# Kernel tuning notes

Hardware: AMD Instinct MI355X
Metric: run time of the kernel (lower is better)

The kernel has to match this reference:

```python
import jax, jax.numpy as jnp
import numpy as np
from jax import lax

C = 256
HEADS = 8
HEAD_DIM = C // HEADS
B, H, W = 16, 32, 32
EPS = 1e-5


def conv3x3(x, w, b):
    # x: [B,C,H,W], w: [O,I,3,3]
    y = lax.conv_general_dilated(x, w, (1, 1), 'SAME',
                                 dimension_numbers=('NCHW', 'OIHW', 'NCHW'))
    return y + b[None, :, None, None]


def conv1x1(x, w, b):
    # w: [O,C]; pointwise conv as einsum
    return jnp.einsum('oc,bchw->bohw', w, x) + b[None, :, None, None]


def batchnorm(x, gamma, beta, mean, var):
    inv = gamma / jnp.sqrt(var + EPS)
    return x * inv[None, :, None, None] + (beta - mean * inv)[None, :, None, None]


def setup_inputs() -> dict:
    key = jax.random.key(0)
    ks = jax.random.split(key, 16)
    s3 = 1.0 / np.sqrt(C * 9)
    s1 = 1.0 / np.sqrt(C)
    return {
        'x': jax.random.normal(ks[0], (B, C, H, W), jnp.float32),
        'conv1_w': jax.random.normal(ks[1], (C, C, 3, 3), jnp.float32) * s3,
        'conv1_b': jnp.zeros((C,), jnp.float32),
        'bn1_gamma': jnp.ones((C,), jnp.float32),
        'bn1_beta': jnp.zeros((C,), jnp.float32),
        'bn1_mean': jax.random.normal(ks[2], (C,), jnp.float32) * 0.1,
        'bn1_var': jax.random.uniform(ks[3], (C,), jnp.float32, 0.5, 1.5),
        'conv2_w': jax.random.normal(ks[4], (C, C, 3, 3), jnp.float32) * s3,
        'conv2_b': jnp.zeros((C,), jnp.float32),
        'bn2_gamma': jnp.ones((C,), jnp.float32),
        'bn2_beta': jnp.zeros((C,), jnp.float32),
        'bn2_mean': jax.random.normal(ks[5], (C,), jnp.float32) * 0.1,
        'bn2_var': jax.random.uniform(ks[6], (C,), jnp.float32, 0.5, 1.5),
        'q_w': jax.random.normal(ks[7], (C, C), jnp.float32) * s1,
        'q_b': jnp.zeros((C,), jnp.float32),
        'k_w': jax.random.normal(ks[8], (C, C), jnp.float32) * s1,
        'k_b': jnp.zeros((C,), jnp.float32),
        'v_w': jax.random.normal(ks[9], (C, C), jnp.float32) * s1,
        'v_b': jnp.zeros((C,), jnp.float32),
        'out_w': jax.random.normal(ks[10], (C, C), jnp.float32) * s1,
        'out_b': jnp.zeros((C,), jnp.float32),
        'gate': jnp.asarray(0.1, jnp.float32),
    }


def reference(x, conv1_w, conv1_b, bn1_gamma, bn1_beta, bn1_mean, bn1_var,
              conv2_w, conv2_b, bn2_gamma, bn2_beta, bn2_mean, bn2_var,
              q_w, q_b, k_w, k_b, v_w, v_b, out_w, out_b, gate):
    b, c, h, w = x.shape
    n = h * w
    residual = x
    # conv residual path
    conv_out = jax.nn.relu(batchnorm(conv3x3(x, conv1_w, conv1_b),
                                     bn1_gamma, bn1_beta, bn1_mean, bn1_var))
    conv_out = batchnorm(conv3x3(conv_out, conv2_w, conv2_b),
                         bn2_gamma, bn2_beta, bn2_mean, bn2_var)
    # spatial multi-head attention (eval mode: dropout is identity)
    q = conv1x1(x, q_w, q_b).reshape(b, HEADS, HEAD_DIM, n)
    k = conv1x1(x, k_w, k_b).reshape(b, HEADS, HEAD_DIM, n)
    v = conv1x1(x, v_w, v_b).reshape(b, HEADS, HEAD_DIM, n)
    scores = jnp.einsum('bhdn,bhdm->bhnm', q, k) / np.sqrt(HEAD_DIM).astype(np.float32)
    attn = jax.nn.softmax(scores, axis=-1)  # [B,heads,N,N]
    attn_out = jnp.einsum('bhdm,bhnm->bhdn', v, attn).reshape(b, c, h, w)
    attn_out = conv1x1(attn_out, out_w, out_b)
    out = conv_out + jax.nn.sigmoid(gate) * attn_out + residual
    return jax.nn.relu(out)
```

## Files before the change

kernel.cpp:

```cpp
#include <hip/hip_runtime.h>
#include <hip/hip_bf16.h>

using bf16 = __hip_bfloat16;
typedef __attribute__((ext_vector_type(4))) float floatx4;
typedef __attribute__((ext_vector_type(8))) __bf16 bf16x8;
typedef __attribute__((ext_vector_type(4))) __bf16 bf16x4;

#define LGKM_WAIT() asm volatile("s_waitcnt lgkmcnt(0)" ::: "memory")

__device__ __forceinline__ void prep_one(const float* __restrict__ src,
                                         bf16* __restrict__ dst, int idx, int ntaps)
{
    const int kk = idx & 31, o = (idx >> 5) & 255, kc = (idx >> 13) & 7, t = idx >> 16;
    dst[idx] = __float2bfloat16(src[(o * 256 + kc * 32 + kk) * ntaps + t]);
}

__global__ __launch_bounds__(256) void prep_all(
    const float* __restrict__ x,
    const float* __restrict__ w1, const float* __restrict__ w2,
    const float* __restrict__ qw, const float* __restrict__ kw,
    const float* __restrict__ vw, const float* __restrict__ ow,
    bf16* __restrict__ xk, bf16* __restrict__ w1f, bf16* __restrict__ w2f,
    bf16* __restrict__ qwf, bf16* __restrict__ kwf,
    bf16* __restrict__ vwf, bf16* __restrict__ owf)
{
    __shared__ float T[64][65];
    const int blk = blockIdx.x, tid = threadIdx.x;
    if (blk < 1024) {
        const int n0 = (blk & 15) * 64, c0 = ((blk >> 4) & 3) * 64, b = blk >> 6;
        #pragma unroll
        for (int it = 0; it < 4; ++it) {
            const int tau = tid + it * 256;
            const int c = tau >> 4, seg = tau & 15;
            const float4 vv = *(const float4*)&x[((b * 256 + c0 + c) << 10) + n0 + seg * 4];
            T[seg * 4 + 0][c] = vv.x; T[seg * 4 + 1][c] = vv.y;
            T[seg * 4 + 2][c] = vv.z; T[seg * 4 + 3][c] = vv.w;
        }
        __syncthreads();
        #pragma unroll
        for (int it = 0; it < 2; ++it) {
            const int tau = tid + it * 256;
            const int n = tau >> 3, seg = tau & 7;
            bf16x8 o8;
            #pragma unroll
            for (int q = 0; q < 8; ++q) o8[q] = (__bf16)T[n][seg * 8 + q];
            const int c = c0 + seg * 8;
            *(bf16x8*)&xk[((((b << 3) + (c >> 5)) << 10) + n0 + n) * 32 + (c & 31)] = o8;
        }
    } else if (blk < 2176) {
        const int base = (blk - 1024) * 256 + tid;
        #pragma unroll
        for (int k = 0; k < 4; ++k) {
            const int idx = base + k * 294912;
            if (idx < 589824) prep_one(w1, w1f, idx, 9);
            else              prep_one(w2, w2f, idx - 589824, 9);
        }
    } else {
        const int r = (blk - 2176) * 256 + tid;
        prep_one(qw, qwf, r, 1);
        prep_one(kw, kwf, r, 1);
        prep_one(vw, vwf, r, 1);
        prep_one(ow, owf, r, 1);
    }
}

template<int MODE>
__global__ __launch_bounds__(256) void conv_k(
    const bf16* __restrict__ Wf, const bf16* __restrict__ Act,
    const float* __restrict__ bias,
    const float* __restrict__ gam, const float* __restrict__ bet,
    const float* __restrict__ mu, const float* __restrict__ var,
    void* __restrict__ outp)
{
    __shared__ __align__(16) unsigned char smb[34816];

    const int bn = blockIdx.x, bo = blockIdx.y, b = blockIdx.z;
    const int tid = threadIdx.x;
    const int wave = tid >> 6, lane = tid & 63;
    const int quad = lane >> 4, l16 = lane & 15;
    const int wm = wave & 1, wn = wave >> 1;

    int srow[4], scol[4], sn[4]; bool sval[4];
    #pragma unroll
    for (int it = 0; it < 4; ++it) {
        const int s = tid + it * 256;
        const int row = s >> 2;
        const int yi = row / 34, x34 = row - yi * 34;
        const int gy = bn * 4 - 1 + yi, gx = x34 - 1;
        sval[it] = (s < 816) & (gy >= 0) & (gy < 32) & (gx >= 0) & (gx < 32);
        sn[it] = (gy << 5) + gx;
        srow[it] = row; scol[it] = (s & 3) * 8;
    }

    const bf16* __restrict__ act0 = Act + ((size_t)b << 18);
    bf16x8 rg[4];
    #pragma unroll
    for (int it = 0; it < 4; ++it) {
        bf16x8 v = {};
        if (sval[it]) v = *(const bf16x8*)&act0[sn[it] * 32 + scol[it]];
        rg[it] = v;
    }
    {
        bf16* st = (bf16*)smb;
        #pragma unroll
        for (int it = 0; it < 4; ++it)
            if (tid + it * 256 < 816) *(bf16x8*)&st[srow[it] * 40 + scol[it]] = rg[it];
    }
    __syncthreads();

    floatx4 acc[4][2] = {};

    for (int kc = 0; kc < 8; ++kc) {
        if (kc < 7) {
            const bf16* __restrict__ actn = act0 + ((kc + 1) << 15);
            #pragma unroll
            for (int it = 0; it < 4; ++it) {
                bf16x8 v = {};
                if (sval[it]) v = *(const bf16x8*)&actn[sn[it] * 32 + scol[it]];
                rg[it] = v;
            }
        }
        const bf16* __restrict__ cur = (const bf16*)(smb + (kc & 1) * 16320);
        #pragma unroll
        for (int t = 0; t < 9; ++t) {
            const int dy = t / 3 - 1, dx = t % 3 - 1;
            bf16x8 af[4], wf[2];
            #pragma unroll
            for (int p = 0; p < 4; ++p) {
                const int m = wm * 64 + p * 16 + l16;
                const int row = ((m >> 5) + 1 + dy) * 34 + ((m & 31) + 1 + dx);
                af[p] = *(const bf16x8*)&cur[row * 40 + quad * 8];
            }
            #pragma unroll
            for (int p = 0; p < 2; ++p)
                wf[p] = *(const bf16x8*)&Wf[((((t * 8 + kc) << 8) + bo * 64 + wn * 32 + p * 16 + l16) << 5) + quad * 8];
            #pragma unroll
            for (int i = 0; i < 4; ++i)
                #pragma unroll
                for (int j = 0; j < 2; ++j)
                    acc[i][j] = __builtin_amdgcn_mfma_f32_16x16x32_bf16(af[i], wf[j], acc[i][j], 0, 0, 0);
        }
        if (kc < 7) {
            bf16* nxt = (bf16*)(smb + ((kc + 1) & 1) * 16320);
            #pragma unroll
            for (int it = 0; it < 4; ++it)
                if (tid + it * 256 < 816) *(bf16x8*)&nxt[srow[it] * 40 + scol[it]] = rg[it];
        }
        __syncthreads();
    }

    if constexpr (MODE == 0) {
        bf16* rp = (bf16*)(smb + wave * 5120);
        #pragma unroll
        for (int i = 0; i < 4; ++i)
            #pragma unroll
            for (int j = 0; j < 2; ++j) {
                const int oc = bo * 64 + wn * 32 + j * 16 + l16;
                const float inv = gam[oc] * rsqrtf(var[oc] + 1e-5f);
                const float sh = bet[oc] - mu[oc] * inv;
                const float bs = bias[oc];
                #pragma unroll
                for (int r = 0; r < 4; ++r) {
                    const float v = (acc[i][j][r] + bs) * inv + sh;
                    rp[(i * 16 + quad * 4 + r) * 40 + j * 16 + l16] =
                        __float2bfloat16(v < 0.0f ? 0.0f : v);
                }
            }
        LGKM_WAIT();
        const int kc2 = bo * 2 + wn;
        bf16* dst = (bf16*)outp + ((((size_t)b << 3) + kc2) << 15) + (bn * 128 + wm * 64) * 32;
        #pragma unroll
        for (int it = 0; it < 4; ++it) {
            const int s = it * 64 + lane;
            const int nl = s >> 2, cp = (s & 3) * 8;
            *(bf16x8*)&dst[nl * 32 + cp] = *(const bf16x8*)&rp[nl * 40 + cp];
        }
    } else {
        float* rp = (float*)(smb + wave * 8704);
        #pragma unroll
        for (int i = 0; i < 4; ++i)
            #pragma unroll
            for (int j = 0; j < 2; ++j) {
                const int oc = bo * 64 + wn * 32 + j * 16 + l16;
                const float inv = gam[oc] * rsqrtf(var[oc] + 1e-5f);
                const float sh = bet[oc] - mu[oc] * inv;
                const float bs = bias[oc];
                float4 o;
                o.x = (acc[i][j][0] + bs) * inv + sh;
                o.y = (acc[i][j][1] + bs) * inv + sh;
                o.z = (acc[i][j][2] + bs) * inv + sh;
                o.w = (acc[i][j][3] + bs) * inv + sh;
                *(float4*)&rp[(j * 16 + l16) * 68 + i * 16 + quad * 4] = o;
            }
        LGKM_WAIT();
        const int n0 = bn * 128 + wm * 64;
        #pragma unroll
        for (int it = 0; it < 8; ++it) {
            const int s = it * 64 + lane;
            const int ocl = s >> 4, nch = s & 15;
            const int oc = bo * 64 + wn * 32 + ocl;
            float4 v = *(const float4*)&rp[ocl * 68 + nch * 4];
            *(float4*)&((float*)outp)[((b * 256 + oc) << 10) + n0 + nch * 4] = v;
        }
    }
}

__global__ __launch_bounds__(256) void qkv_k(
    const bf16* __restrict__ Wq, const bf16* __restrict__ Wk, const bf16* __restrict__ Wv,
    const bf16* __restrict__ Act,
    const float* __restrict__ bq, const float* __restrict__ bk, const float* __restrict__ bv,
    bf16* __restrict__ Oq, bf16* __restrict__ Ok, bf16* __restrict__ Ov, float qscale)
{
    __shared__ __align__(16) unsigned char qsm[20480];
    const int bn = blockIdx.x, by = blockIdx.y, b = blockIdx.z;
    const int sel = by >> 2, bo = by & 3;
    const bf16* __restrict__ Wf = (sel == 0) ? Wq : (sel == 1) ? Wk : Wv;
    const float* __restrict__ bias = (sel == 0) ? bq : (sel == 1) ? bk : bv;
    const float scale = (sel == 0) ? qscale : 1.0f;

    const int tid = threadIdx.x;
    const int wave = tid >> 6, lane = tid & 63;
    const int quad = lane >> 4, l16 = lane & 15;
    const int wm = wave & 1, wn = wave >> 1;

    floatx4 acc[4][2] = {};

    for (int kc = 0; kc < 8; ++kc) {
        const bf16* __restrict__ actk = Act + ((size_t)b << 18) + (kc << 15);
        bf16x8 af[4], wf[2];
        #pragma unroll
        for (int p = 0; p < 4; ++p)
            af[p] = *(const bf16x8*)&actk[(bn * 128 + wm * 64 + p * 16 + l16) * 32 + quad * 8];
        #pragma unroll
        for (int p = 0; p < 2; ++p)
            wf[p] = *(const bf16x8*)&Wf[(((kc << 8) + bo * 64 + wn * 32 + p * 16 + l16) << 5) + quad * 8];
        #pragma unroll
        for (int i = 0; i < 4; ++i)
            #pragma unroll
            for (int j = 0; j < 2; ++j)
                acc[i][j] = __builtin_amdgcn_mfma_f32_16x16x32_bf16(af[i], wf[j], acc[i][j], 0, 0, 0);
    }

    if (sel < 2) {
        bf16* rp = (bf16*)(qsm + wave * 5120);
        #pragma unroll
        for (int i = 0; i < 4; ++i)
            #pragma unroll
            for (int j = 0; j < 2; ++j) {
                const int oc = bo * 64 + wn * 32 + j * 16 + l16;
                const float bs = bias[oc];
                #pragma unroll
                for (int r = 0; r < 4; ++r)
                    rp[(i * 16 + quad * 4 + r) * 40 + j * 16 + l16] =
                        __float2bfloat16((acc[i][j][r] + bs) * scale);
            }
        LGKM_WAIT();
        bf16* __restrict__ outp = (sel == 0) ? Oq : Ok;
        const int h = bo * 2 + wn;
        bf16* dst = outp + ((((size_t)b << 3) + h) << 15) + (bn * 128 + wm * 64) * 32;
        #pragma unroll
        for (int it = 0; it < 4; ++it) {
            const int s = it * 64 + lane;
            const int nl = s >> 2, cp = (s & 3) * 8;
            *(bf16x8*)&dst[nl * 32 + cp] = *(const bf16x8*)&rp[nl * 40 + cp];
        }
    } else {
        bf16* rp = (bf16*)(qsm + wave * 4608);
        #pragma unroll
        for (int i = 0; i < 4; ++i)
            #pragma unroll
            for (int j = 0; j < 2; ++j) {
                const int oc = bo * 64 + wn * 32 + j * 16 + l16;
                const float bs = bias[oc];
                bf16x4 o4;
                #pragma unroll
                for (int r = 0; r < 4; ++r) o4[r] = (__bf16)(acc[i][j][r] + bs);
                *(bf16x4*)&rp[(j * 16 + l16) * 72 + i * 16 + quad * 4] = o4;
            }
        LGKM_WAIT();
        const int n0 = bn * 128 + wm * 64;
        #pragma unroll
        for (int it = 0; it < 4; ++it) {
            const int s = it * 64 + lane;
            const int ocl = s >> 3, nch = s & 7;
            const int oc = bo * 64 + wn * 32 + ocl;
            *(bf16x8*)&Ov[((b * 256 + oc) << 10) + n0 + nch * 8] =
                *(const bf16x8*)&rp[ocl * 72 + nch * 8];
        }
    }
}

__global__ __launch_bounds__(256) void attn_kernel(
    const bf16* __restrict__ Q, const bf16* __restrict__ K,
    const bf16* __restrict__ V, bf16* __restrict__ O)
{
    __shared__ __align__(16) bf16 Pl[4][32][136];

    const int qb = blockIdx.x, h = blockIdx.y, b = blockIdx.z;
    const int tid = threadIdx.x;
    const int wave = tid >> 6, lane = tid & 63;
    const int quad = lane >> 4, l16 = lane & 15;

    const bf16* __restrict__ Qh = Q + ((((size_t)b << 3) + h) << 15);
    const bf16* __restrict__ Kh = K + ((((size_t)b << 3) + h) << 15);
    const int qrow0 = qb * 128 + wave * 32;

    bf16x8 qf[2];
    #pragma unroll
    for (int i = 0; i < 2; ++i)
        qf[i] = *(const bf16x8*)&Qh[(qrow0 + i * 16 + l16) * 32 + quad * 8];

    float lp[2] = {0.0f, 0.0f};
    floatx4 oacc[2][2] = {};

    for (int kt = 0; kt < 8; ++kt) {
        bf16x8 kf[8];
        #pragma unroll
        for (int kb = 0; kb < 8; ++kb)
            kf[kb] = *(const bf16x8*)&Kh[(kt * 128 + kb * 16 + l16) * 32 + quad * 8];
        bf16x8 vb[2][4];
        #pragma unroll
        for (int jd = 0; jd < 2; ++jd)
            #pragma unroll
            for (int kk = 0; kk < 4; ++kk)
                vb[jd][kk] = *(const bf16x8*)&V[((b * 256 + h * 32 + jd * 16 + l16) << 10)
                                               + kt * 128 + kk * 32 + quad * 8];

        #pragma unroll
        for (int kb = 0; kb < 8; ++kb) {
            #pragma unroll
            for (int i = 0; i < 2; ++i) {
                floatx4 zz = {0.f, 0.f, 0.f, 0.f};
                floatx4 st = __builtin_amdgcn_mfma_f32_16x16x32_bf16(kf[kb], qf[i], zz, 0, 0, 0);
                const float e0 = __expf(st[0]), e1 = __expf(st[1]);
                const float e2 = __expf(st[2]), e3 = __expf(st[3]);
                lp[i] += (e0 + e1) + (e2 + e3);
                bf16x4 p4 = {(__bf16)e0, (__bf16)e1, (__bf16)e2, (__bf16)e3};
                *(bf16x4*)&Pl[wave][i * 16 + l16][kb * 16 + quad * 4] = p4;
            }
        }

        #pragma unroll
        for (int kk = 0; kk < 4; ++kk) {
            bf16x8 pf[2];
            #pragma unroll
            for (int i = 0; i < 2; ++i)
                pf[i] = *(const bf16x8*)&Pl[wave][i * 16 + l16][kk * 32 + quad * 8];
            #pragma unroll
            for (int jd = 0; jd < 2; ++jd)
                #pragma unroll
                for (int i = 0; i < 2; ++i)
                    oacc[jd][i] = __builtin_amdgcn_mfma_f32_16x16x32_bf16(
                        vb[jd][kk], pf[i], oacc[jd][i], 0, 0, 0);
        }
    }

    bf16* __restrict__ Oh = O + ((((size_t)b << 3) + h) << 15);
    #pragma unroll
    for (int i = 0; i < 2; ++i) {
        float l = lp[i];
        l += __shfl_xor(l, 16, 64);
        l += __shfl_xor(l, 32, 64);
        const float inv = 1.0f / l;
        const int qn = qrow0 + i * 16 + l16;
        #pragma unroll
        for (int jd = 0; jd < 2; ++jd) {
            bf16x4 o4;
            #pragma unroll
            for (int r = 0; r < 4; ++r) o4[r] = (__bf16)(oacc[jd][i][r] * inv);
            *(bf16x4*)&Oh[qn * 32 + jd * 16 + quad * 4] = o4;
        }
    }
}

__global__ __launch_bounds__(256) void fi_k(
    const bf16* __restrict__ Wf, const bf16* __restrict__ Act,
    const float* __restrict__ bias,
    const float* __restrict__ c2, const float* __restrict__ resid,
    const float* __restrict__ gate, float* __restrict__ outp)
{
    __shared__ __align__(16) unsigned char fsm[34816];
    const int bn = blockIdx.x, bo = blockIdx.y, b = blockIdx.z;
    const int tid = threadIdx.x;
    const int wave = tid >> 6, lane = tid & 63;
    const int quad = lane >> 4, l16 = lane & 15;
    const int wm = wave & 1, wn = wave >> 1;

    floatx4 acc[4][2] = {};

    for (int kc = 0; kc < 8; ++kc) {
        const bf16* __restrict__ actk = Act + ((size_t)b << 18) + (kc << 15);
        bf16x8 af[4], wf[2];
        #pragma unroll
        for (int p = 0; p < 4; ++p)
            af[p] = *(const bf16x8*)&actk[(bn * 128 + wm * 64 + p * 16 + l16) * 32 + quad * 8];
        #pragma unroll
        for (int p = 0; p < 2; ++p)
            wf[p] = *(const bf16x8*)&Wf[(((kc << 8) + bo * 64 + wn * 32 + p * 16 + l16) << 5) + quad * 8];
        #pragma unroll
        for (int i = 0; i < 4; ++i)
            #pragma unroll
            for (int j = 0; j < 2; ++j)
                acc[i][j] = __builtin_amdgcn_mfma_f32_16x16x32_bf16(af[i], wf[j], acc[i][j], 0, 0, 0);
    }

    const float sg = 1.0f / (1.0f + __expf(-gate[0]));

    float* rp = (float*)(fsm + wave * 8704);
    #pragma unroll
    for (int i = 0; i < 4; ++i)
        #pragma unroll
        for (int j = 0; j < 2; ++j) {
            const int oc = bo * 64 + wn * 32 + j * 16 + l16;
            const float bs = bias[oc];
            float4 o;
            o.x = acc[i][j][0] + bs; o.y = acc[i][j][1] + bs;
            o.z = acc[i][j][2] + bs; o.w = acc[i][j][3] + bs;
            *(float4*)&rp[(j * 16 + l16) * 68 + i * 16 + quad * 4] = o;
        }
    LGKM_WAIT();
    const int n0 = bn * 128 + wm * 64;
    #pragma unroll
    for (int it = 0; it < 8; ++it) {
        const int s = it * 64 + lane;
        const int ocl = s >> 4, nch = s & 15;
        const int oc = bo * 64 + wn * 32 + ocl;
        const int idx = ((b * 256 + oc) << 10) + n0 + nch * 4;
        float4 v = *(const float4*)&rp[ocl * 68 + nch * 4];
        const float4 cc = *(const float4*)&c2[idx];
        const float4 rr = *(const float4*)&resid[idx];
        float4 o;
        o.x = cc.x + sg * v.x + rr.x; o.y = cc.y + sg * v.y + rr.y;
        o.z = cc.z + sg * v.z + rr.z; o.w = cc.w + sg * v.w + rr.w;
        o.x = o.x < 0.0f ? 0.0f : o.x; o.y = o.y < 0.0f ? 0.0f : o.y;
        o.z = o.z < 0.0f ? 0.0f : o.z; o.w = o.w < 0.0f ? 0.0f : o.w;
        *(float4*)&outp[idx] = o;
    }
}

extern "C" void kernel_launch(void* const* d_in, const int* in_sizes, int n_in,
                              void* d_out, int out_size, void* d_ws, size_t ws_size,
                              hipStream_t stream)
{
    const float* x    = (const float*)d_in[0];
    const float* w1   = (const float*)d_in[1];
    const float* cb1  = (const float*)d_in[2];
    const float* g1   = (const float*)d_in[3];
    const float* be1  = (const float*)d_in[4];
    const float* mu1  = (const float*)d_in[5];
    const float* va1  = (const float*)d_in[6];
    const float* w2   = (const float*)d_in[7];
    const float* cb2  = (const float*)d_in[8];
    const float* g2   = (const float*)d_in[9];
    const float* be2  = (const float*)d_in[10];
    const float* mu2  = (const float*)d_in[11];
    const float* va2  = (const float*)d_in[12];
    const float* qw   = (const float*)d_in[13];
    const float* qb_  = (const float*)d_in[14];
    const float* kw   = (const float*)d_in[15];
    const float* kb_  = (const float*)d_in[16];
    const float* vw   = (const float*)d_in[17];
    const float* vb_  = (const float*)d_in[18];
    const float* ow   = (const float*)d_in[19];
    const float* ob_  = (const float*)d_in[20];
    const float* gate = (const float*)d_in[21];

    char* ws = (char*)d_ws;
    bf16*  xk    = (bf16*) (ws + 0);
    bf16*  y1k   = (bf16*) (ws + 8388608);
    bf16*  attnk = (bf16*) (ws + 8388608);
    float* c2    = (float*)(ws + 16777216);
    bf16*  qT    = (bf16*) (ws + 33554432);
    bf16*  kT    = (bf16*) (ws + 41943040);
    bf16*  vbuf  = (bf16*) (ws + 50331648);
    bf16*  w1f   = (bf16*) (ws + 58720256);
    bf16*  w2f   = (bf16*) (ws + 59899904);
    bf16*  qwf   = (bf16*) (ws + 61079552);
    bf16*  kwf   = (bf16*) (ws + 61210624);
    bf16*  vwf   = (bf16*) (ws + 61341696);
    bf16*  owf   = (bf16*) (ws + 61472768);

    dim3 blk(256, 1, 1);
    prep_all<<<dim3(2432), blk, 0, stream>>>(x, w1, w2, qw, kw, vw, ow,
                                             xk, w1f, w2f, qwf, kwf, vwf, owf);

    dim3 gg(8, 4, 16);
    conv_k<0><<<gg, blk, 0, stream>>>(w1f, xk, cb1, g1, be1, mu1, va1, (void*)y1k);
    conv_k<1><<<gg, blk, 0, stream>>>(w2f, y1k, cb2, g2, be2, mu2, va2, (void*)c2);
    qkv_k<<<dim3(8, 12, 16), blk, 0, stream>>>(qwf, kwf, vwf, xk, qb_, kb_, vb_,
                                               qT, kT, vbuf, 0.17677669529663687f);
    attn_kernel<<<dim3(8, 8, 16), blk, 0, stream>>>(qT, kT, vbuf, attnk);
    fi_k<<<gg, blk, 0, stream>>>(owf, attnk, ob_, c2, x, gate, (float*)d_out);

    (void)in_sizes; (void)n_in; (void)out_size; (void)ws_size;
}
```

Measured before the change: 262.0 us.

## Halve per-block tiles, remap blocks across XCDs, prefetch conv weights, use exp2

The conv, out-projection and attention kernels now use half-size tiles: the conv covers 2 rows instead of 4 and attention handles 16 query rows per wave instead of 32. This doubles the block count, which raises occupancy and fills the GPU better. Blocks launch on a 1D grid and are remapped so each XCD handles a fixed set of batches, aiming for better L2 locality. The conv loop prefetches the next tap's weights from global memory during the current tap's MFMAs. Attention switches to exp2 with log2(e) folded into the Q scale. In exchange, halo and weight reloads per output element increase.

```diff
diff --git a/kernel.cpp b/kernel.cpp
--- a/kernel.cpp
+++ b/kernel.cpp
@@ -7,6 +7,14 @@
 typedef __attribute__((ext_vector_type(4))) __bf16 bf16x4;
 
 #define LGKM_WAIT() asm volatile("s_waitcnt lgkmcnt(0)" ::: "memory")
+
+__device__ __forceinline__ void remap1024(int L, int& bn, int& bo, int& b)
+{
+    const int xcd = L & 7, slot = L >> 3;
+    b  = (xcd << 1) | (slot & 1);
+    bo = (slot >> 1) & 3;
+    bn = slot >> 3;
+}
 
 __device__ __forceinline__ void prep_one(const float* __restrict__ src,
                                          bf16* __restrict__ dst, int idx, int ntaps)
@@ -72,30 +80,30 @@
     const float* __restrict__ mu, const float* __restrict__ var,
     void* __restrict__ outp)
 {
-    __shared__ __align__(16) unsigned char smb[34816];
-
-    const int bn = blockIdx.x, bo = blockIdx.y, b = blockIdx.z;
+    __shared__ __align__(16) unsigned char smb[21760];
+
+    int bn, bo, b; remap1024(blockIdx.x, bn, bo, b);
     const int tid = threadIdx.x;
     const int wave = tid >> 6, lane = tid & 63;
     const int quad = lane >> 4, l16 = lane & 15;
     const int wm = wave & 1, wn = wave >> 1;
 
-    int srow[4], scol[4], sn[4]; bool sval[4];
+    int srow[3], scol[3], sn[3]; bool sval[3];
     #pragma unroll
-    for (int it = 0; it < 4; ++it) {
+    for (int it = 0; it < 3; ++it) {
         const int s = tid + it * 256;
         const int row = s >> 2;
         const int yi = row / 34, x34 = row - yi * 34;
-        const int gy = bn * 4 - 1 + yi, gx = x34 - 1;
-        sval[it] = (s < 816) & (gy >= 0) & (gy < 32) & (gx >= 0) & (gx < 32);
+        const int gy = bn * 2 - 1 + yi, gx = x34 - 1;
+        sval[it] = (s < 544) & (gy >= 0) & (gy < 32) & (gx >= 0) & (gx < 32);
         sn[it] = (gy << 5) + gx;
         srow[it] = row; scol[it] = (s & 3) * 8;
     }
 
     const bf16* __restrict__ act0 = Act + ((size_t)b << 18);
-    bf16x8 rg[4];
+    bf16x8 rg[3];
     #pragma unroll
-    for (int it = 0; it < 4; ++it) {
+    for (int it = 0; it < 3; ++it) {
         bf16x8 v = {};
         if (sval[it]) v = *(const bf16x8*)&act0[sn[it] * 32 + scol[it]];
         rg[it] = v;
@@ -103,56 +111,67 @@
     {
         bf16* st = (bf16*)smb;
         #pragma unroll
-        for (int it = 0; it < 4; ++it)
-            if (tid + it * 256 < 816) *(bf16x8*)&st[srow[it] * 40 + scol[it]] = rg[it];
+        for (int it = 0; it < 3; ++it)
+            if (tid + it * 256 < 544) *(bf16x8*)&st[srow[it] * 40 + scol[it]] = rg[it];
     }
     __syncthreads();
 
-    floatx4 acc[4][2] = {};
+    floatx4 acc[2][2] = {};
+
+    bf16x8 wcur[2];
+    #pragma unroll
+    for (int p = 0; p < 2; ++p)
+        wcur[p] = *(const bf16x8*)&Wf[(((0 * 8 + 0) << 8) + bo * 64 + wn * 32 + p * 16 + l16) * 32 + quad * 8];
 
     for (int kc = 0; kc < 8; ++kc) {
         if (kc < 7) {
             const bf16* __restrict__ actn = act0 + ((kc + 1) << 15);
             #pragma unroll
-            for (int it = 0; it < 4; ++it) {
+            for (int it = 0; it < 3; ++it) {
                 bf16x8 v = {};
                 if (sval[it]) v = *(const bf16x8*)&actn[sn[it] * 32 + scol[it]];
                 rg[it] = v;
             }
         }
-        const bf16* __restrict__ cur = (const bf16*)(smb + (kc & 1) * 16320);
+        const bf16* __restrict__ cur = (const bf16*)(smb + (kc & 1) * 10880);
         #pragma unroll
         for (int t = 0; t < 9; ++t) {
+            const int nt  = (t == 8) ? 0 : t + 1;
+            const int nkc = (t == 8) ? kc + 1 : kc;
+            bf16x8 wnxt[2] = {};
+            if (nkc < 8) {
+                #pragma unroll
+                for (int p = 0; p < 2; ++p)
+                    wnxt[p] = *(const bf16x8*)&Wf[(((nt * 8 + nkc) << 8) + bo * 64 + wn * 32 + p * 16 + l16) * 32 + quad * 8];
+            }
             const int dy = t / 3 - 1, dx = t % 3 - 1;
-            bf16x8 af[4], wf[2];
-            #pragma unroll
-            for (int p = 0; p < 4; ++p) {
-                const int m = wm * 64 + p * 16 + l16;
+            bf16x8 af[2];
+            #pragma unroll
+            for (int p = 0; p < 2; ++p) {
+                const int m = wm * 32 + p * 16 + l16;
                 const int row = ((m >> 5) + 1 + dy) * 34 + ((m & 31) + 1 + dx);
                 af[p] = *(const bf16x8*)&cur[row * 40 + quad * 8];
             }
             #pragma unroll
-            for (int p = 0; p < 2; ++p)
-                wf[p] = *(const bf16x8*)&Wf[((((t * 8 + kc) << 8) + bo * 64 + wn * 32 + p * 16 + l16) << 5) + quad * 8];
-            #pragma unroll
-            for (int i = 0; i < 4; ++i)
+            for (int i = 0; i < 2; ++i)
                 #pragma unroll
                 for (int j = 0; j < 2; ++j)
-                    acc[i][j] = __builtin_amdgcn_mfma_f32_16x16x32_bf16(af[i], wf[j], acc[i][j], 0, 0, 0);
+                    acc[i][j] = __builtin_amdgcn_mfma_f32_16x16x32_bf16(af[i], wcur[j], acc[i][j], 0, 0, 0);
+            wcur[0] = wnxt[0]; wcur[1] = wnxt[1];
         }
         if (kc < 7) {
-            bf16* nxt = (bf16*)(smb + ((kc + 1) & 1) * 16320);
-            #pragma unroll
-            for (int it = 0; it < 4; ++it)
-                if (tid + it * 256 < 816) *(bf16x8*)&nxt[srow[it] * 40 + scol[it]] = rg[it];
+            bf16* nxt = (bf16*)(smb + ((kc + 1) & 1) * 10880);
+            #pragma unroll
+            for (int it = 0; it < 3; ++it)
+                if (tid + it * 256 < 544) *(bf16x8*)&nxt[srow[it] * 40 + scol[it]] = rg[it];
         }
         __syncthreads();
     }
 
     if constexpr (MODE == 0) {
-        bf16* rp = (bf16*)(smb + wave * 5120);
-        #pragma unroll
-        for (int i = 0; i < 4; ++i)
+        bf16* rp = (bf16*)(smb + wave * 2560);
+        #pragma unroll
+        for (int i = 0; i < 2; ++i)
             #pragma unroll
             for (int j = 0; j < 2; ++j) {
                 const int oc = bo * 64 + wn * 32 + j * 16 + l16;
@@ -168,17 +187,17 @@
             }
         LGKM_WAIT();
         const int kc2 = bo * 2 + wn;
-        bf16* dst = (bf16*)outp + ((((size_t)b << 3) + kc2) << 15) + (bn * 128 + wm * 64) * 32;
-        #pragma unroll
-        for (int it = 0; it < 4; ++it) {
+        bf16* dst = (bf16*)outp + ((((size_t)b << 3) + kc2) << 15) + (bn * 64 + wm * 32) * 32;
+        #pragma unroll
+        for (int it = 0; it < 2; ++it) {
             const int s = it * 64 + lane;
             const int nl = s >> 2, cp = (s & 3) * 8;
             *(bf16x8*)&dst[nl * 32 + cp] = *(const bf16x8*)&rp[nl * 40 + cp];
         }
     } else {
-        float* rp = (float*)(smb + wave * 8704);
-        #pragma unroll
-        for (int i = 0; i < 4; ++i)
+        float* rp = (float*)(smb + wave * 4608);
+        #pragma unroll
+        for (int i = 0; i < 2; ++i)
             #pragma unroll
             for (int j = 0; j < 2; ++j) {
                 const int oc = bo * 64 + wn * 32 + j * 16 + l16;
@@ -190,16 +209,16 @@
                 o.y = (acc[i][j][1] + bs) * inv + sh;
                 o.z = (acc[i][j][2] + bs) * inv + sh;
                 o.w = (acc[i][j][3] + bs) * inv + sh;
-                *(float4*)&rp[(j * 16 + l16) * 68 + i * 16 + quad * 4] = o;
+                *(float4*)&rp[(j * 16 + l16) * 36 + i * 16 + quad * 4] = o;
             }
         LGKM_WAIT();
-        const int n0 = bn * 128 + wm * 64;
-        #pragma unroll
-        for (int it = 0; it < 8; ++it) {
+        const int n0 = bn * 64 + wm * 32;
+        #pragma unroll
+        for (int it = 0; it < 4; ++it) {
             const int s = it * 64 + lane;
-            const int ocl = s >> 4, nch = s & 15;
+            const int ocl = s >> 3, nch = s & 7;
             const int oc = bo * 64 + wn * 32 + ocl;
-            float4 v = *(const float4*)&rp[ocl * 68 + nch * 4];
+            float4 v = *(const float4*)&rp[ocl * 36 + nch * 4];
             *(float4*)&((float*)outp)[((b * 256 + oc) << 10) + n0 + nch * 4] = v;
         }
     }
@@ -212,7 +231,11 @@
     bf16* __restrict__ Oq, bf16* __restrict__ Ok, bf16* __restrict__ Ov, float qscale)
 {
     __shared__ __align__(16) unsigned char qsm[20480];
-    const int bn = blockIdx.x, by = blockIdx.y, b = blockIdx.z;
+    const int L = blockIdx.x;
+    const int xcd = L & 7, slot = L >> 3;
+    const int b = (xcd << 1) | (slot & 1);
+    const int s1 = slot >> 1;
+    const int by = s1 % 12, bn = s1 / 12;
     const int sel = by >> 2, bo = by & 3;
     const bf16* __restrict__ Wf = (sel == 0) ? Wq : (sel == 1) ? Wk : Wv;
     const float* __restrict__ bias = (sel == 0) ? bq : (sel == 1) ? bk : bv;
@@ -294,24 +317,23 @@
     const bf16* __restrict__ Q, const bf16* __restrict__ K,
     const bf16* __restrict__ V, bf16* __restrict__ O)
 {
-    __shared__ __align__(16) bf16 Pl[4][32][136];
-
-    const int qb = blockIdx.x, h = blockIdx.y, b = blockIdx.z;
+    __shared__ __align__(16) bf16 Pl[4][16][136];
+
+    const int L = blockIdx.x;
+    const int h = L & 7, slot = L >> 3;
+    const int b = slot & 15, qb = slot >> 4;
     const int tid = threadIdx.x;
     const int wave = tid >> 6, lane = tid & 63;
     const int quad = lane >> 4, l16 = lane & 15;
 
     const bf16* __restrict__ Qh = Q + ((((size_t)b << 3) + h) << 15);
     const bf16* __restrict__ Kh = K + ((((size_t)b << 3) + h) << 15);
-    const int qrow0 = qb * 128 + wave * 32;
-
-    bf16x8 qf[2];
-    #pragma unroll
-    for (int i = 0; i < 2; ++i)
-        qf[i] = *(const bf16x8*)&Qh[(qrow0 + i * 16 + l16) * 32 + quad * 8];
-
-    float lp[2] = {0.0f, 0.0f};
-    floatx4 oacc[2][2] = {};
+    const int qrow0 = qb * 64 + wave * 16;
+
+    bf16x8 qf = *(const bf16x8*)&Qh[(qrow0 + l16) * 32 + quad * 8];
+
+    float lp = 0.0f;
+    floatx4 oacc[2] = {};
 
     for (int kt = 0; kt < 8; ++kt) {
         bf16x8 kf[8];
@@ -328,48 +350,38 @@
 
         #pragma unroll
         for (int kb = 0; kb < 8; ++kb) {
-            #pragma unroll
-            for (int i = 0; i < 2; ++i) {
-                floatx4 zz = {0.f, 0.f, 0.f, 0.f};
-                floatx4 st = __builtin_amdgcn_mfma_f32_16x16x32_bf16(kf[kb], qf[i], zz, 0, 0, 0);
-                const float e0 = __expf(st[0]), e1 = __expf(st[1]);
-                const float e2 = __expf(st[2]), e3 = __expf(st[3]);
-                lp[i] += (e0 + e1) + (e2 + e3);
-                bf16x4 p4 = {(__bf16)e0, (__bf16)e1, (__bf16)e2, (__bf16)e3};
-                *(bf16x4*)&Pl[wave][i * 16 + l16][kb * 16 + quad * 4] = p4;
-            }
+            floatx4 zz = {0.f, 0.f, 0.f, 0.f};
+            floatx4 st = __builtin_amdgcn_mfma_f32_16x16x32_bf16(kf[kb], qf, zz, 0, 0, 0);
+            const float e0 = __builtin_amdgcn_exp2f(st[0]);
+            const float e1 = __builtin_amdgcn_exp2f(st[1]);
+            const float e2 = __builtin_amdgcn_exp2f(st[2]);
+            const float e3 = __builtin_amdgcn_exp2f(st[3]);
+            lp += (e0 + e1) + (e2 + e3);
+            bf16x4 p4 = {(__bf16)e0, (__bf16)e1, (__bf16)e2, (__bf16)e3};
+            *(bf16x4*)&Pl[wave][l16][kb * 16 + quad * 4] = p4;
         }
 
         #pragma unroll
         for (int kk = 0; kk < 4; ++kk) {
-            bf16x8 pf[2];
-            #pragma unroll
-            for (int i = 0; i < 2; ++i)
-                pf[i] = *(const bf16x8*)&Pl[wave][i * 16 + l16][kk * 32 + quad * 8];
+            bf16x8 pf = *(const bf16x8*)&Pl[wave][l16][kk * 32 + quad * 8];
             #pragma unroll
             for (int jd = 0; jd < 2; ++jd)
-                #pragma unroll
-                for (int i = 0; i < 2; ++i)
-                    oacc[jd][i] = __builtin_amdgcn_mfma_f32_16x16x32_bf16(
-                        vb[jd][kk], pf[i], oacc[jd][i], 0, 0, 0);
-        }
-    }
-
+                oacc[jd] = __builtin_amdgcn_mfma_f32_16x16x32_bf16(vb[jd][kk], pf, oacc[jd], 0, 0, 0);
+        }
+    }
+
+    float l = lp;
+    l += __shfl_xor(l, 16, 64);
+    l += __shfl_xor(l, 32, 64);
+    const float inv = 1.0f / l;
     bf16* __restrict__ Oh = O + ((((size_t)b << 3) + h) << 15);
+    const int qn = qrow0 + l16;
     #pragma unroll
-    for (int i = 0; i < 2; ++i) {
-        float l = lp[i];
-        l += __shfl_xor(l, 16, 64);
-        l += __shfl_xor(l, 32, 64);
-        const float inv = 1.0f / l;
-        const int qn = qrow0 + i * 16 + l16;
-        #pragma unroll
-        for (int jd = 0; jd < 2; ++jd) {
-            bf16x4 o4;
-            #pragma unroll
-            for (int r = 0; r < 4; ++r) o4[r] = (__bf16)(oacc[jd][i][r] * inv);
-            *(bf16x4*)&Oh[qn * 32 + jd * 16 + quad * 4] = o4;
-        }
+    for (int jd = 0; jd < 2; ++jd) {
+        bf16x4 o4;
+        #pragma unroll
+        for (int r = 0; r < 4; ++r) o4[r] = (__bf16)(oacc[jd][r] * inv);
+        *(bf16x4*)&Oh[qn * 32 + jd * 16 + quad * 4] = o4;
     }
 }
 
@@ -379,26 +391,26 @@
     const float* __restrict__ c2, const float* __restrict__ resid,
     const float* __restrict__ gate, float* __restrict__ outp)
 {
-    __shared__ __align__(16) unsigned char fsm[34816];
-    const int bn = blockIdx.x, bo = blockIdx.y, b = blockIdx.z;
+    __shared__ __align__(16) unsigned char fsm[18432];
+    int bn, bo, b; remap1024(blockIdx.x, bn, bo, b);
     const int tid = threadIdx.x;
     const int wave = tid >> 6, lane = tid & 63;
     const int quad = lane >> 4, l16 = lane & 15;
     const int wm = wave & 1, wn = wave >> 1;
 
-    floatx4 acc[4][2] = {};
+    floatx4 acc[2][2] = {};
 
     for (int kc = 0; kc < 8; ++kc) {
         const bf16* __restrict__ actk = Act + ((size_t)b << 18) + (kc << 15);
-        bf16x8 af[4], wf[2];
-        #pragma unroll
-        for (int p = 0; p < 4; ++p)
-            af[p] = *(const bf16x8*)&actk[(bn * 128 + wm * 64 + p * 16 + l16) * 32 + quad * 8];
+        bf16x8 af[2], wf[2];
+        #pragma unroll
+        for (int p = 0; p < 2; ++p)
+            af[p] = *(const bf16x8*)&actk[(bn * 64 + wm * 32 + p * 16 + l16) * 32 + quad * 8];
         #pragma unroll
         for (int p = 0; p < 2; ++p)
             wf[p] = *(const bf16x8*)&Wf[(((kc << 8) + bo * 64 + wn * 32 + p * 16 + l16) << 5) + quad * 8];
         #pragma unroll
-        for (int i = 0; i < 4; ++i)
+        for (int i = 0; i < 2; ++i)
             #pragma unroll
             for (int j = 0; j < 2; ++j)
                 acc[i][j] = __builtin_amdgcn_mfma_f32_16x16x32_bf16(af[i], wf[j], acc[i][j], 0, 0, 0);
@@ -406,9 +418,9 @@
 
     const float sg = 1.0f / (1.0f + __expf(-gate[0]));
 
-    float* rp = (float*)(fsm + wave * 8704);
+    float* rp = (float*)(fsm + wave * 4608);
     #pragma unroll
-    for (int i = 0; i < 4; ++i)
+    for (int i = 0; i < 2; ++i)
         #pragma unroll
         for (int j = 0; j < 2; ++j) {
             const int oc = bo * 64 + wn * 32 + j * 16 + l16;
@@ -416,17 +428,17 @@
             float4 o;
             o.x = acc[i][j][0] + bs; o.y = acc[i][j][1] + bs;
             o.z = acc[i][j][2] + bs; o.w = acc[i][j][3] + bs;
-            *(float4*)&rp[(j * 16 + l16) * 68 + i * 16 + quad * 4] = o;
+            *(float4*)&rp[(j * 16 + l16) * 36 + i * 16 + quad * 4] = o;
         }
     LGKM_WAIT();
-    const int n0 = bn * 128 + wm * 64;
+    const int n0 = bn * 64 + wm * 32;
     #pragma unroll
-    for (int it = 0; it < 8; ++it) {
+    for (int it = 0; it < 4; ++it) {
         const int s = it * 64 + lane;
-        const int ocl = s >> 4, nch = s & 15;
+        const int ocl = s >> 3, nch = s & 7;
         const int oc = bo * 64 + wn * 32 + ocl;
         const int idx = ((b * 256 + oc) << 10) + n0 + nch * 4;
-        float4 v = *(const float4*)&rp[ocl * 68 + nch * 4];
+        float4 v = *(const float4*)&rp[ocl * 36 + nch * 4];
         const float4 cc = *(const float4*)&c2[idx];
         const float4 rr = *(const float4*)&resid[idx];
         float4 o;
@@ -484,13 +496,12 @@
     prep_all<<<dim3(2432), blk, 0, stream>>>(x, w1, w2, qw, kw, vw, ow,
                                              xk, w1f, w2f, qwf, kwf, vwf, owf);
 
-    dim3 gg(8, 4, 16);
-    conv_k<0><<<gg, blk, 0, stream>>>(w1f, xk, cb1, g1, be1, mu1, va1, (void*)y1k);
-    conv_k<1><<<gg, blk, 0, stream>>>(w2f, y1k, cb2, g2, be2, mu2, va2, (void*)c2);
-    qkv_k<<<dim3(8, 12, 16), blk, 0, stream>>>(qwf, kwf, vwf, xk, qb_, kb_, vb_,
-                                               qT, kT, vbuf, 0.17677669529663687f);
-    attn_kernel<<<dim3(8, 8, 16), blk, 0, stream>>>(qT, kT, vbuf, attnk);
-    fi_k<<<gg, blk, 0, stream>>>(owf, attnk, ob_, c2, x, gate, (float*)d_out);
+    conv_k<0><<<dim3(1024), blk, 0, stream>>>(w1f, xk, cb1, g1, be1, mu1, va1, (void*)y1k);
+    conv_k<1><<<dim3(1024), blk, 0, stream>>>(w2f, y1k, cb2, g2, be2, mu2, va2, (void*)c2);
+    qkv_k<<<dim3(1536), blk, 0, stream>>>(qwf, kwf, vwf, xk, qb_, kb_, vb_,
+                                          qT, kT, vbuf, 0.2550392430300696f);
+    attn_kernel<<<dim3(2048), blk, 0, stream>>>(qT, kT, vbuf, attnk);
+    fi_k<<<dim3(1024), blk, 0, stream>>>(owf, attnk, ob_, c2, x, gate, (float*)d_out);
 
     (void)in_sizes; (void)n_in; (void)out_size; (void)ws_size;
 }
```

Result: slower. 310.8 us (+18.6%).
